# Performance work log

Hardware: AMD Instinct MI355X
Metric: run time of the kernel (lower is better)

## Reference

```python
import jax, jax.numpy as jnp
import numpy as np

B, S, D, H = 4, 2048, 1024, 16
DK = D // H

def setup_inputs() -> dict:
    key = jax.random.key(0)
    ks = jax.random.split(key, 8)
    scale = 1.0 / np.sqrt(D)
    return {
        "q": jax.random.normal(ks[0], (B, S, D), jnp.float32),
        "k": jax.random.normal(ks[1], (B, S, D), jnp.float32),
        "v": jax.random.normal(ks[2], (B, S, D), jnp.float32),
        "wq": jax.random.normal(ks[3], (D, D), jnp.float32) * scale,
        "bq": jnp.zeros((D,), jnp.float32),
        "wk": jax.random.normal(ks[4], (D, D), jnp.float32) * scale,
        "bk": jnp.zeros((D,), jnp.float32),
        "wv": jax.random.normal(ks[5], (D, D), jnp.float32) * scale,
        "bv": jnp.zeros((D,), jnp.float32),
        "wo": jax.random.normal(ks[6], (D, D), jnp.float32) * scale,
        "bo": jnp.zeros((D,), jnp.float32),
    }

def reference(q, k, v, wq, bq, wk, bk, wv, bv, wo, bo):
    b, s, _ = q.shape
    # projections; split heads -> [b, h, s, d_k]
    def proj(x, w, bias):
        y = x @ w + bias
        return y.reshape(b, -1, H, DK).transpose(0, 2, 1, 3)
    qh, kh, vh = proj(q, wq, bq), proj(k, wk, bk), proj(v, wv, bv)
    scores = jnp.einsum("bhqd,bhkd->bhqk", qh, kh) / np.sqrt(DK).astype(jnp.float32)
    attn = jax.nn.softmax(scores, axis=-1)  # dropout = identity (eval mode)
    out = jnp.einsum("bhqk,bhkd->bhqd", attn, vh)
    out = out.transpose(0, 2, 1, 3).reshape(b, s, D)
    return out @ wo + bo
```

## Files before the change

### kernel.cpp

```cpp
#include <hip/hip_runtime.h>
#include <hip/hip_bf16.h>

#define B_   4
#define S_   2048
#define D_   1024
#define H_   16
#define DK_  64
#define NTOK 8192

typedef __bf16 bf16_t;
typedef __bf16 bf16x8 __attribute__((ext_vector_type(8)));
typedef __bf16 bf16x4 __attribute__((ext_vector_type(4)));
typedef __bf16 bf16x2 __attribute__((ext_vector_type(2)));
typedef float  f32x4  __attribute__((ext_vector_type(4)));
typedef float  f32x16 __attribute__((ext_vector_type(16)));
typedef unsigned u32x4 __attribute__((ext_vector_type(4)));
typedef int    i32x2  __attribute__((ext_vector_type(2)));

__device__ __forceinline__ void gll16(const void* g, void* l) {
  __builtin_amdgcn_global_load_lds(
      (const __attribute__((address_space(1))) void*)g,
      (__attribute__((address_space(3))) void*)l,
      16, 0, 0);
}

__device__ __forceinline__ f32x4 mfma32(bf16x8 a, bf16x8 b, f32x4 c) {
  return __builtin_amdgcn_mfma_f32_16x16x32_bf16(a, b, c, 0, 0, 0);
}

__device__ __forceinline__ f32x16 mfma32x32(bf16x8 a, bf16x8 b, f32x16 c) {
#if defined(__HIP_DEVICE_COMPILE__)
  return __builtin_amdgcn_mfma_f32_32x32x16_bf16(a, b, c, 0, 0, 0);
#else
  (void)a; (void)b;
  return c;
#endif
}

__device__ __forceinline__ float fast_exp2(float x) {
#if defined(__HIP_DEVICE_COMPILE__) && __has_builtin(__builtin_amdgcn_exp2f)
  return __builtin_amdgcn_exp2f(x);
#else
  return exp2f(x);
#endif
}

__device__ __forceinline__ f32x16 zero16() {
  f32x16 z;
#pragma unroll
  for (int i = 0; i < 16; ++i) z[i] = 0.f;
  return z;
}

__device__ __forceinline__ unsigned pkbf(float lo, float hi) {
  bf16x2 t;
  t[0] = (bf16_t)lo;
  t[1] = (bf16_t)hi;
  return __builtin_bit_cast(unsigned, t);
}

__device__ __forceinline__ void plswap(unsigned &x, unsigned &y) {
#if defined(__HIP_DEVICE_COMPILE__)
  i32x2 r = __builtin_amdgcn_permlane32_swap((int)x, (int)y, false, false);
  x = (unsigned)r[0];
  y = (unsigned)r[1];
#endif
}

__device__ __forceinline__ void build_pa(const f32x16 s, bf16x8 &p0, bf16x8 &p1) {
  unsigned A0 = pkbf(fast_exp2(s[0]),  fast_exp2(s[1]));
  unsigned A1 = pkbf(fast_exp2(s[2]),  fast_exp2(s[3]));
  unsigned B0 = pkbf(fast_exp2(s[4]),  fast_exp2(s[5]));
  unsigned B1 = pkbf(fast_exp2(s[6]),  fast_exp2(s[7]));
  unsigned C0 = pkbf(fast_exp2(s[8]),  fast_exp2(s[9]));
  unsigned C1 = pkbf(fast_exp2(s[10]), fast_exp2(s[11]));
  unsigned D0 = pkbf(fast_exp2(s[12]), fast_exp2(s[13]));
  unsigned D1 = pkbf(fast_exp2(s[14]), fast_exp2(s[15]));
  plswap(A0, B0);
  plswap(A1, B1);
  plswap(C0, D0);
  plswap(C1, D1);
  u32x4 lo = {A0, A1, B0, B1};
  u32x4 hi = {C0, C1, D0, D1};
  p0 = __builtin_bit_cast(bf16x8, lo);
  p1 = __builtin_bit_cast(bf16x8, hi);
}

__global__ __launch_bounds__(256) void tobf16(
    const float* __restrict__ q, const float* __restrict__ k,
    const float* __restrict__ v, bf16_t* __restrict__ o) {
  const float* src = (blockIdx.z == 0) ? q : (blockIdx.z == 1) ? k : v;
  bf16_t* dst = o + (size_t)blockIdx.z * 8388608;
  size_t i = ((size_t)blockIdx.x * 256 + threadIdx.x) * 4;
  float4 x = *(const float4*)&src[i];
  bf16x4 y;
  y[0] = (bf16_t)x.x; y[1] = (bf16_t)x.y;
  y[2] = (bf16_t)x.z; y[3] = (bf16_t)x.w;
  *(bf16x4*)&dst[i] = y;
}

__global__ __launch_bounds__(256) void prep_weights(
    const float* __restrict__ wq, const float* __restrict__ wk,
    const float* __restrict__ wv, const float* __restrict__ wo,
    bf16_t* __restrict__ wtHi) {
  const int z = blockIdx.z;
  const float* W = (z == 0) ? wq : (z == 1) ? wk : (z == 2) ? wv : wo;
  const int k0 = blockIdx.x * 64;
  const int n0 = blockIdx.y * 64;
  const int t = threadIdx.x;
  __shared__ float T[64][65];
#pragma unroll
  for (int rr = 0; rr < 4; ++rr) {
    int row = rr * 16 + (t >> 4);
    int cc = (t & 15) * 4;
    const float4 v = *(const float4*)&W[(size_t)(k0 + row) * D_ + n0 + cc];
    T[row][cc + 0] = v.x; T[row][cc + 1] = v.y;
    T[row][cc + 2] = v.z; T[row][cc + 3] = v.w;
  }
  __syncthreads();
  const int n = t >> 2;
  const int kc = (t & 3) * 16;
  bf16x8 h0, h1;
#pragma unroll
  for (int j = 0; j < 16; ++j) {
    float vv = T[kc + j][n];
    if (j < 8) h0[j] = (bf16_t)vv;
    else       h1[j - 8] = (bf16_t)vv;
  }
  size_t ofs = (size_t)z * 1048576 + (size_t)(n0 + n) * D_ + k0 + kc;
  *(bf16x8*)&wtHi[ofs] = h0; *(bf16x8*)&wtHi[ofs + 8] = h1;
}

__global__ __launch_bounds__(256) void gemm_qkv_bf16(
    const bf16_t* __restrict__ Abf,
    const float* __restrict__ bq, const float* __restrict__ bk,
    const float* __restrict__ bv,
    const bf16_t* __restrict__ wtHi, bf16_t* __restrict__ outQKV) {
  const int z = blockIdx.z;
  const bf16_t* A   = Abf + (size_t)z * 8388608;
  const float* bias = (z == 0) ? bq : (z == 1) ? bk : bv;
  const bf16_t* WHi = wtHi + (size_t)z * 1048576;
  bf16_t* Out = outQKV + (size_t)z * 8388608;

  const int row0 = blockIdx.x * 128;
  const int col0 = blockIdx.y * 128;
  const int t = threadIdx.x;
  const int w = t >> 6, L = t & 63;
  const int m = L & 15, g = L >> 4;

  __shared__ __align__(16) bf16_t As2[128 * 32];
  __shared__ __align__(16) bf16_t Whi_s[128 * 32];

  f32x4 acc[4][4];
#pragma unroll
  for (int i = 0; i < 4; ++i)
#pragma unroll
    for (int j = 0; j < 4; ++j) acc[i][j] = (f32x4){0.f, 0.f, 0.f, 0.f};

  const int aw0 = (w & 1) * 64;
  const int bw0 = (w >> 1) * 64;

  for (int kt = 0; kt < 32; ++kt) {
    const int k0 = kt * 32;
#pragma unroll
    for (int rr = 0; rr < 2; ++rr) {
      int lin16 = rr * 256 + t;
      int n = lin16 >> 2;
      int c = (lin16 & 3) ^ ((n >> 1) & 3);
      gll16(&A[(size_t)(row0 + n) * D_ + k0 + c * 8], &As2[rr * 2048 + w * 512]);
      gll16(&WHi[(size_t)(col0 + n) * D_ + k0 + c * 8], &Whi_s[rr * 2048 + w * 512]);
    }
    __syncthreads();

    bf16x8 af[4], wh[4];
#pragma unroll
    for (int it = 0; it < 4; ++it) {
      int row = aw0 + it * 16 + m;
      int sl = (g ^ ((m >> 1) & 3)) * 8;
      af[it] = *(const bf16x8*)&As2[row * 32 + sl];
    }
#pragma unroll
    for (int jt = 0; jt < 4; ++jt) {
      int n = bw0 + jt * 16 + m;
      int sl = (g ^ ((m >> 1) & 3)) * 8;
      wh[jt] = *(const bf16x8*)&Whi_s[n * 32 + sl];
    }
#pragma unroll
    for (int it = 0; it < 4; ++it)
#pragma unroll
      for (int jt = 0; jt < 4; ++jt)
        acc[it][jt] = mfma32(af[it], wh[jt], acc[it][jt]);
    __syncthreads();
  }
#pragma unroll
  for (int jt = 0; jt < 4; ++jt) {
    int col = col0 + bw0 + jt * 16 + m;
    float bcol = bias[col];
    int h = col >> 6, d = col & 63;
#pragma unroll
    for (int it = 0; it < 4; ++it) {
      if (z != 2) {
#pragma unroll
        for (int r = 0; r < 4; ++r) {
          int row = row0 + aw0 + it * 16 + g * 4 + r;
          int b = row >> 11, s = row & 2047;
          Out[((size_t)((b * H_ + h) * S_ + s)) * DK_ + d] =
              (bf16_t)(acc[it][jt][r] + bcol);
        }
      } else {
        int row = row0 + aw0 + it * 16 + g * 4;
        int b = row >> 11, s = row & 2047;
        bf16x4 p4;
#pragma unroll
        for (int r = 0; r < 4; ++r) p4[r] = (bf16_t)(acc[it][jt][r] + bcol);
        *(bf16x4*)&Out[((size_t)((b * H_ + h) * DK_ + d)) * S_ + s] = p4;
      }
    }
  }
}

__global__ __launch_bounds__(256) void gemm_qkv_f32(
    const float* __restrict__ Aq, const float* __restrict__ Ak,
    const float* __restrict__ Av,
    const float* __restrict__ bq, const float* __restrict__ bk,
    const float* __restrict__ bv,
    const bf16_t* __restrict__ wtHi, bf16_t* __restrict__ outQKV) {
  const int z = blockIdx.z;
  const float* A    = (z == 0) ? Aq : (z == 1) ? Ak : Av;
  const float* bias = (z == 0) ? bq : (z == 1) ? bk : bv;
  const bf16_t* WHi = wtHi + (size_t)z * 1048576;
  bf16_t* Out = outQKV + (size_t)z * 8388608;

  const int row0 = blockIdx.x * 128;
  const int col0 = blockIdx.y * 128;
  const int t = threadIdx.x;
  const int w = t >> 6, L = t & 63;
  const int m = L & 15, g = L >> 4;

  __shared__ __align__(16) float  As[128 * 32];
  __shared__ __align__(16) bf16_t Whi_s[128 * 32];

  f32x4 acc[4][4];
#pragma unroll
  for (int i = 0; i < 4; ++i)
#pragma unroll
    for (int j = 0; j < 4; ++j) acc[i][j] = (f32x4){0.f, 0.f, 0.f, 0.f};

  const int aw0 = (w & 1) * 64;
  const int bw0 = (w >> 1) * 64;

  for (int kt = 0; kt < 32; ++kt) {
    const int k0 = kt * 32;
#pragma unroll
    for (int rr = 0; rr < 4; ++rr) {
      int lin16 = rr * 256 + t;
      int row = lin16 >> 3;
      int c = (lin16 & 7) ^ (row & 7);
      gll16(&A[(size_t)(row0 + row) * D_ + k0 + c * 4], &As[rr * 1024 + w * 256]);
    }
#pragma unroll
    for (int rr = 0; rr < 2; ++rr) {
      int lin16 = rr * 256 + t;
      int n = lin16 >> 2;
      int c = (lin16 & 3) ^ ((n >> 1) & 3);
      gll16(&WHi[(size_t)(col0 + n) * D_ + k0 + c * 8], &Whi_s[rr * 2048 + w * 512]);
    }
    __syncthreads();

    bf16x8 af[4], wh[4];
#pragma unroll
    for (int it = 0; it < 4; ++it) {
      int row = aw0 + it * 16 + m;
      const f32x4* p = (const f32x4*)&As[row * 32];
      f32x4 x0 = p[(2 * g) ^ (m & 7)];
      f32x4 x1 = p[(2 * g + 1) ^ (m & 7)];
      bf16x8 a;
      a[0] = (bf16_t)x0.x; a[1] = (bf16_t)x0.y; a[2] = (bf16_t)x0.z; a[3] = (bf16_t)x0.w;
      a[4] = (bf16_t)x1.x; a[5] = (bf16_t)x1.y; a[6] = (bf16_t)x1.z; a[7] = (bf16_t)x1.w;
      af[it] = a;
    }
#pragma unroll
    for (int jt = 0; jt < 4; ++jt) {
      int n = bw0 + jt * 16 + m;
      int sl = (g ^ ((m >> 1) & 3)) * 8;
      wh[jt] = *(const bf16x8*)&Whi_s[n * 32 + sl];
    }
#pragma unroll
    for (int it = 0; it < 4; ++it)
#pragma unroll
      for (int jt = 0; jt < 4; ++jt)
        acc[it][jt] = mfma32(af[it], wh[jt], acc[it][jt]);
    __syncthreads();
  }
#pragma unroll
  for (int jt = 0; jt < 4; ++jt) {
    int col = col0 + bw0 + jt * 16 + m;
    float bcol = bias[col];
    int h = col >> 6, d = col & 63;
#pragma unroll
    for (int it = 0; it < 4; ++it) {
      if (z != 2) {
#pragma unroll
        for (int r = 0; r < 4; ++r) {
          int row = row0 + aw0 + it * 16 + g * 4 + r;
          int b = row >> 11, s = row & 2047;
          Out[((size_t)((b * H_ + h) * S_ + s)) * DK_ + d] =
              (bf16_t)(acc[it][jt][r] + bcol);
        }
      } else {
        int row = row0 + aw0 + it * 16 + g * 4;
        int b = row >> 11, s = row & 2047;
        bf16x4 p4;
#pragma unroll
        for (int r = 0; r < 4; ++r) p4[r] = (bf16_t)(acc[it][jt][r] + bcol);
        *(bf16x4*)&Out[((size_t)((b * H_ + h) * DK_ + d)) * S_ + s] = p4;
      }
    }
  }
}

__global__ __launch_bounds__(256, 2) void attn(
    const bf16_t* __restrict__ Qh, const bf16_t* __restrict__ Kh,
    const bf16_t* __restrict__ VhT, bf16_t* __restrict__ Ohi) {
  const int bh = blockIdx.y;
  const int q0 = blockIdx.x * 128;
  const int t = threadIdx.x, w = t >> 6;
  const int lane = t & 63;
  const int lo5 = lane & 31, hi = lane >> 5;

  __shared__ __align__(16) bf16_t Ks[64 * 64];
  __shared__ __align__(16) bf16_t Vt[64 * 64];

  const size_t qbase = (size_t)bh * S_ * DK_;
  const size_t vbase = (size_t)bh * DK_ * S_;

  const int qrow = q0 + w * 32 + lo5;
  bf16x8 qf[4];
#pragma unroll
  for (int ks = 0; ks < 4; ++ks) {
    bf16x8 v = *(const bf16x8*)&Qh[qbase + (size_t)qrow * DK_ + ks * 16 + hi * 8];
#pragma unroll
    for (int j = 0; j < 8; ++j) v[j] = (bf16_t)(0.18033688f * (float)v[j]);
    qf[ks] = v;
  }

  bf16x8 ones;
#pragma unroll
  for (int j = 0; j < 8; ++j) ones[j] = (bf16_t)1.f;

  int offs[4];
#pragma unroll
  for (int ks = 0; ks < 4; ++ks)
    offs[ks] = lo5 * 64 + (((ks * 2 + hi) ^ (lo5 & 7)) * 8);

  f32x16 oacc0 = zero16(), oacc1 = zero16(), lacc = zero16();

  for (int kv0 = 0; kv0 < S_; kv0 += 64) {
#pragma unroll
    for (int rr = 0; rr < 2; ++rr) {
      int lin16 = rr * 256 + t;
      int rrow = lin16 >> 3;
      int c = (lin16 & 7) ^ (rrow & 7);
      gll16(&Kh[qbase + (size_t)(kv0 + rrow) * DK_ + c * 8], &Ks[rr * 2048 + w * 512]);
      gll16(&VhT[vbase + (size_t)rrow * S_ + kv0 + c * 8], &Vt[rr * 2048 + w * 512]);
    }
    __syncthreads();

    f32x16 sc0 = zero16(), sc1 = zero16();
#pragma unroll
    for (int ks = 0; ks < 4; ++ks) {
      bf16x8 k0 = *(const bf16x8*)&Ks[offs[ks]];
      bf16x8 k1 = *(const bf16x8*)&Ks[offs[ks] + 2048];
      sc0 = mfma32x32(k0, qf[ks], sc0);
      sc1 = mfma32x32(k1, qf[ks], sc1);
    }

    bf16x8 pa0, pa1, pa2, pa3;
    build_pa(sc0, pa0, pa1);
    build_pa(sc1, pa2, pa3);

#pragma unroll
    for (int ks = 0; ks < 4; ++ks) {
      bf16x8 pb = (ks == 0) ? pa0 : (ks == 1) ? pa1 : (ks == 2) ? pa2 : pa3;
      lacc = mfma32x32(ones, pb, lacc);
      bf16x8 v0 = *(const bf16x8*)&Vt[offs[ks]];
      bf16x8 v1 = *(const bf16x8*)&Vt[offs[ks] + 2048];
      oacc0 = mfma32x32(v0, pb, oacc0);
      oacc1 = mfma32x32(v1, pb, oacc1);
    }
    __syncthreads();
  }

  const int b = bh >> 4, h = bh & 15;
  const float inv = 1.f / lacc[0];
  const size_t rowofs = ((size_t)(b * S_ + qrow)) * D_ + h * DK_;
#pragma unroll
  for (int rg = 0; rg < 4; ++rg) {
    bf16x4 o0, o1;
#pragma unroll
    for (int j = 0; j < 4; ++j) {
      o0[j] = (bf16_t)(oacc0[rg * 4 + j] * inv);
      o1[j] = (bf16_t)(oacc1[rg * 4 + j] * inv);
    }
    *(bf16x4*)&Ohi[rowofs + rg * 8 + hi * 4] = o0;
    *(bf16x4*)&Ohi[rowofs + 32 + rg * 8 + hi * 4] = o1;
  }
}

__global__ __launch_bounds__(256) void gemm_out(
    const bf16_t* __restrict__ Ahi, const bf16_t* __restrict__ wtHi,
    const float* __restrict__ bias, float* __restrict__ Out) {
  const bf16_t* WHi = wtHi + (size_t)3 * 1048576;
  const int row0 = blockIdx.x * 128;
  const int col0 = blockIdx.y * 128;
  const int t = threadIdx.x;
  const int w = t >> 6, L = t & 63;
  const int m = L & 15, g = L >> 4;

  __shared__ __align__(16) bf16_t Ahi_s[128 * 32];
  __shared__ __align__(16) bf16_t Whi_s[128 * 32];

  f32x4 acc[4][4];
#pragma unroll
  for (int i = 0; i < 4; ++i)
#pragma unroll
    for (int j = 0; j < 4; ++j) acc[i][j] = (f32x4){0.f, 0.f, 0.f, 0.f};

  const int aw0 = (w & 1) * 64;
  const int bw0 = (w >> 1) * 64;

  for (int kt = 0; kt < 32; ++kt) {
    const int k0 = kt * 32;
#pragma unroll
    for (int rr = 0; rr < 2; ++rr) {
      int lin16 = rr * 256 + t;
      int n = lin16 >> 2;
      int c = (lin16 & 3) ^ ((n >> 1) & 3);
      gll16(&Ahi[(size_t)(row0 + n) * D_ + k0 + c * 8], &Ahi_s[rr * 2048 + w * 512]);
      gll16(&WHi[(size_t)(col0 + n) * D_ + k0 + c * 8], &Whi_s[rr * 2048 + w * 512]);
    }
    __syncthreads();

    bf16x8 ah[4], wh[4];
#pragma unroll
    for (int it = 0; it < 4; ++it) {
      int row = aw0 + it * 16 + m;
      int sl = (g ^ ((m >> 1) & 3)) * 8;
      ah[it] = *(const bf16x8*)&Ahi_s[row * 32 + sl];
    }
#pragma unroll
    for (int jt = 0; jt < 4; ++jt) {
      int n = bw0 + jt * 16 + m;
      int sl = (g ^ ((m >> 1) & 3)) * 8;
      wh[jt] = *(const bf16x8*)&Whi_s[n * 32 + sl];
    }
#pragma unroll
    for (int it = 0; it < 4; ++it)
#pragma unroll
      for (int jt = 0; jt < 4; ++jt)
        acc[it][jt] = mfma32(ah[it], wh[jt], acc[it][jt]);
    __syncthreads();
  }
#pragma unroll
  for (int jt = 0; jt < 4; ++jt) {
    int col = col0 + bw0 + jt * 16 + m;
    float bcol = bias[col];
#pragma unroll
    for (int it = 0; it < 4; ++it)
#pragma unroll
      for (int r = 0; r < 4; ++r) {
        int row = row0 + aw0 + it * 16 + g * 4 + r;
        Out[(size_t)row * D_ + col] = acc[it][jt][r] + bcol;
      }
  }
}

extern "C" void kernel_launch(void* const* d_in, const int* in_sizes, int n_in,
                              void* d_out, int out_size, void* d_ws, size_t ws_size,
                              hipStream_t stream) {
  const float* q  = (const float*)d_in[0];
  const float* k  = (const float*)d_in[1];
  const float* v  = (const float*)d_in[2];
  const float* wq = (const float*)d_in[3];
  const float* bq = (const float*)d_in[4];
  const float* wk = (const float*)d_in[5];
  const float* bk = (const float*)d_in[6];
  const float* wv = (const float*)d_in[7];
  const float* bv = (const float*)d_in[8];
  const float* wo = (const float*)d_in[9];
  const float* bo = (const float*)d_in[10];
  float* out = (float*)d_out;

  char* ws = (char*)d_ws;
  bf16_t* wtHi = (bf16_t*)(ws);
  bf16_t* QKVh = (bf16_t*)(ws + (8ull << 20));
  bf16_t* Ohi  = (bf16_t*)(ws + (56ull << 20));
  bf16_t* Abf  = (bf16_t*)(ws + (56ull << 20));

  const bool big = ws_size >= (104ull << 20);

  hipLaunchKernelGGL(prep_weights, dim3(16, 16, 4), dim3(256), 0, stream,
                     wq, wk, wv, wo, wtHi);
  if (big) {
    hipLaunchKernelGGL(tobf16, dim3(8192, 1, 3), dim3(256), 0, stream,
                       q, k, v, Abf);
    hipLaunchKernelGGL(gemm_qkv_bf16, dim3(64, 8, 3), dim3(256), 0, stream,
                       Abf, bq, bk, bv, wtHi, QKVh);
  } else {
    hipLaunchKernelGGL(gemm_qkv_f32, dim3(64, 8, 3), dim3(256), 0, stream,
                       q, k, v, bq, bk, bv, wtHi, QKVh);
  }
  hipLaunchKernelGGL(attn, dim3(16, 64), dim3(256), 0, stream,
                     QKVh, QKVh + 8388608, QKVh + 16777216, Ohi);
  hipLaunchKernelGGL(gemm_out, dim3(64, 8), dim3(256), 0, stream,
                     Ohi, wtHi, bo, out);
}
```

Baseline: 350.2 us.

## Double-buffer K/V tiles in attention and swizzle block-to-head mapping

The attention kernel now keeps two LDS buffers for K and V and issues the global-to-LDS loads for the next 64-key tile before computing on the current one. This drops one barrier per iteration and lets load latency overlap with the MFMA work. The block index is also remapped so that consecutive blocks land on different heads, which may spread L2 traffic differently. LDS use doubles to 32KB per block, which can limit occupancy beyond the two blocks per CU that the launch bounds assume. The single barrier per iteration still guards the buffer swap correctly.

```diff
diff --git a/kernel.cpp b/kernel.cpp
--- a/kernel.cpp
+++ b/kernel.cpp
@@ -322,18 +322,40 @@
 __global__ __launch_bounds__(256, 2) void attn(
     const bf16_t* __restrict__ Qh, const bf16_t* __restrict__ Kh,
     const bf16_t* __restrict__ VhT, bf16_t* __restrict__ Ohi) {
-  const int bh = blockIdx.y;
-  const int q0 = blockIdx.x * 128;
+  const int lin = blockIdx.y * 16 + blockIdx.x;
+  const int swz = (lin & 7) * 128 + (lin >> 3);
+  const int bh = swz >> 4;
+  const int q0 = (swz & 15) * 128;
+
   const int t = threadIdx.x, w = t >> 6;
   const int lane = t & 63;
   const int lo5 = lane & 31, hi = lane >> 5;
 
-  __shared__ __align__(16) bf16_t Ks[64 * 64];
-  __shared__ __align__(16) bf16_t Vt[64 * 64];
+  __shared__ __align__(16) bf16_t Ks[2][64 * 64];
+  __shared__ __align__(16) bf16_t Vt[2][64 * 64];
 
   const size_t qbase = (size_t)bh * S_ * DK_;
   const size_t vbase = (size_t)bh * DK_ * S_;
 
+  const int lin16a = t, lin16b = 256 + t;
+  const int rowa = lin16a >> 3, rowb = lin16b >> 3;
+  const int ca = (lin16a & 7) ^ (rowa & 7);
+  const int cb = (lin16b & 7) ^ (rowb & 7);
+
+#define STAGE(buf, kv0)                                                        \
+  do {                                                                         \
+    gll16(&Kh[qbase + (size_t)((kv0) + rowa) * DK_ + ca * 8],                  \
+          &Ks[buf][w * 512]);                                                  \
+    gll16(&VhT[vbase + (size_t)rowa * S_ + (kv0) + ca * 8],                    \
+          &Vt[buf][w * 512]);                                                  \
+    gll16(&Kh[qbase + (size_t)((kv0) + rowb) * DK_ + cb * 8],                  \
+          &Ks[buf][2048 + w * 512]);                                           \
+    gll16(&VhT[vbase + (size_t)rowb * S_ + (kv0) + cb * 8],                    \
+          &Vt[buf][2048 + w * 512]);                                           \
+  } while (0)
+
+  STAGE(0, 0);
+
   const int qrow = q0 + w * 32 + lo5;
   bf16x8 qf[4];
 #pragma unroll
@@ -355,22 +377,20 @@
 
   f32x16 oacc0 = zero16(), oacc1 = zero16(), lacc = zero16();
 
-  for (int kv0 = 0; kv0 < S_; kv0 += 64) {
-#pragma unroll
-    for (int rr = 0; rr < 2; ++rr) {
-      int lin16 = rr * 256 + t;
-      int rrow = lin16 >> 3;
-      int c = (lin16 & 7) ^ (rrow & 7);
-      gll16(&Kh[qbase + (size_t)(kv0 + rrow) * DK_ + c * 8], &Ks[rr * 2048 + w * 512]);
-      gll16(&VhT[vbase + (size_t)rrow * S_ + kv0 + c * 8], &Vt[rr * 2048 + w * 512]);
-    }
-    __syncthreads();
+  __syncthreads();
+
+  for (int it = 0; it < 32; ++it) {
+    const int cur = it & 1;
+    if (it < 31) STAGE(cur ^ 1, (it + 1) * 64);
+
+    const bf16_t* ks_b = &Ks[cur][0];
+    const bf16_t* vt_b = &Vt[cur][0];
 
     f32x16 sc0 = zero16(), sc1 = zero16();
 #pragma unroll
     for (int ks = 0; ks < 4; ++ks) {
-      bf16x8 k0 = *(const bf16x8*)&Ks[offs[ks]];
-      bf16x8 k1 = *(const bf16x8*)&Ks[offs[ks] + 2048];
+      bf16x8 k0 = *(const bf16x8*)&ks_b[offs[ks]];
+      bf16x8 k1 = *(const bf16x8*)&ks_b[offs[ks] + 2048];
       sc0 = mfma32x32(k0, qf[ks], sc0);
       sc1 = mfma32x32(k1, qf[ks], sc1);
     }
@@ -383,13 +403,15 @@
     for (int ks = 0; ks < 4; ++ks) {
       bf16x8 pb = (ks == 0) ? pa0 : (ks == 1) ? pa1 : (ks == 2) ? pa2 : pa3;
       lacc = mfma32x32(ones, pb, lacc);
-      bf16x8 v0 = *(const bf16x8*)&Vt[offs[ks]];
-      bf16x8 v1 = *(const bf16x8*)&Vt[offs[ks] + 2048];
+      bf16x8 v0 = *(const bf16x8*)&vt_b[offs[ks]];
+      bf16x8 v1 = *(const bf16x8*)&vt_b[offs[ks] + 2048];
       oacc0 = mfma32x32(v0, pb, oacc0);
       oacc1 = mfma32x32(v1, pb, oacc1);
     }
-    __syncthreads();
-  }
+
+    __syncthreads();
+  }
+#undef STAGE
 
   const int b = bh >> 4, h = bh & 15;
   const float inv = 1.f / lacc[0];
```

Result: no change. 348.6 us (-0.5%).
